# Kernel optimization log

Measured on AMD Instinct MI355X. Metric: run time of the kernel, lower is better.

The kernel has to match this reference:

```python
import jax, jax.numpy as jnp
import numpy as np

D_MODEL = 1024
D_Q = 1024
D_V = 1024


def setup_inputs() -> dict:
    key = jax.random.key(0)
    k0, k1, k2, k3 = jax.random.split(key, 4)
    embedding_word = jax.random.normal(k0, (4, 2048, D_MODEL), dtype=jnp.float32)
    # nn.Linear weights are [out, in]; we store transposed [in, out] for x @ W
    s = 1.0 / np.sqrt(D_MODEL)
    w_q = jax.random.uniform(k1, (D_MODEL, D_Q), jnp.float32, -s, s)
    w_k = jax.random.uniform(k2, (D_MODEL, D_Q), jnp.float32, -s, s)
    w_v = jax.random.uniform(k3, (D_MODEL, D_V), jnp.float32, -s, s)
    return {"embedding_word": embedding_word, "w_q": w_q, "w_k": w_k, "w_v": w_v}


def reference(embedding_word, w_q, w_k, w_v):
    # q,k: [B,T,d_q]; v: [B,T,d_v]
    q = embedding_word @ w_q
    k = embedding_word @ w_k
    v = embedding_word @ w_v
    scores = jnp.einsum("btd,bsd->bts", q, k)  # [B,T,T]
    T = scores.shape[-1]
    causal = jnp.tril(jnp.ones((T, T), dtype=bool))  # True = keep
    masked = jnp.where(causal, scores, -jnp.inf)
    weights = jax.nn.softmax(masked / jnp.sqrt(jnp.float32(D_Q)), axis=-1)
    return jnp.einsum("bts,bsv->btv", weights, v)
```

## Files before the change

kernel.cpp:

```cpp
#include <hip/hip_runtime.h>
#include <cstdint>

typedef __bf16 bf16_t;
typedef __attribute__((ext_vector_type(8))) __bf16 bf16x8;
typedef __attribute__((ext_vector_type(4))) __bf16 bf16x4;
typedef __attribute__((ext_vector_type(4))) float f32x4;

#define AS1 __attribute__((address_space(1)))
#define AS3 __attribute__((address_space(3)))

template <typename OutT>
__global__ __launch_bounds__(256)
void gemm_nt(const bf16_t* __restrict__ A, const bf16_t* __restrict__ B,
             OutT* __restrict__ C, int K, int lda, int ldb, int ldc,
             long sA, long sB, long sC, int causalSkip, int kLimit)
{
  int bm = blockIdx.y;
  const int bn = blockIdx.x;
  if (kLimit) bm = gridDim.y - 1 - bm;
  if (causalSkip && bn > bm) return;
  A += (long)blockIdx.z * sA;
  B += (long)blockIdx.z * sB;
  C += (long)blockIdx.z * sC;
  const int m0 = bm * 128, n0 = bn * 128;
  int Keff = K;
  if (kLimit) { const int kl = (bm + 1) * 128; if (kl < Keff) Keff = kl; }

  __shared__ bf16_t As[128 * 64];
  __shared__ bf16_t Bs[128 * 64];

  const int tid = threadIdx.x;
  const int wave = tid >> 6, lane = tid & 63;
  const int lm = lane & 15, qd = lane >> 4;
  const int wm = (wave >> 1) * 64, wn = (wave & 1) * 64;

  const int rowl = lane >> 3;
  const int q = (lane & 7) ^ rowl;
  const bf16_t* Abase = A + (long)(m0 + wave * 8 + rowl) * lda + q * 8;
  const bf16_t* Bbase = B + (long)(n0 + wave * 8 + rowl) * ldb + q * 8;
  bf16_t* AsW = As + wave * 512;
  bf16_t* BsW = Bs + wave * 512;

  f32x4 acc[4][4] = {};

  for (int k0 = 0; k0 < Keff; k0 += 64) {
#pragma unroll
    for (int i = 0; i < 4; i++) {
      __builtin_amdgcn_global_load_lds((const AS1 void*)(Abase + (long)i * 32 * lda + k0),
                                       (AS3 void*)(AsW + i * 2048), 16, 0, 0);
      __builtin_amdgcn_global_load_lds((const AS1 void*)(Bbase + (long)i * 32 * ldb + k0),
                                       (AS3 void*)(BsW + i * 2048), 16, 0, 0);
    }
    __syncthreads();
#pragma unroll
    for (int s = 0; s < 2; s++) {
      bf16x8 aF[4], bF[4];
#pragma unroll
      for (int i = 0; i < 4; i++) {
        const int r = wm + i * 16 + lm;
        aF[i] = *(const bf16x8*)&As[r * 64 + (((s * 4 + qd) ^ (lm & 7)) << 3)];
      }
#pragma unroll
      for (int j = 0; j < 4; j++) {
        const int r = wn + j * 16 + lm;
        bF[j] = *(const bf16x8*)&Bs[r * 64 + (((s * 4 + qd) ^ (lm & 7)) << 3)];
      }
#pragma unroll
      for (int i = 0; i < 4; i++)
#pragma unroll
        for (int j = 0; j < 4; j++)
          acc[i][j] = __builtin_amdgcn_mfma_f32_16x16x32_bf16(aF[i], bF[j], acc[i][j], 0, 0, 0);
    }
    __syncthreads();
  }

#pragma unroll
  for (int i = 0; i < 4; i++) {
    const int row = m0 + wm + i * 16 + qd * 4;
#pragma unroll
    for (int j = 0; j < 4; j++) {
      const int col = n0 + wn + j * 16 + lm;
#pragma unroll
      for (int r = 0; r < 4; r++)
        C[(long)(row + r) * ldc + col] = (OutT)acc[i][j][r];
    }
  }
}

__global__ void cvt_f32_bf16(const float* __restrict__ in, bf16_t* __restrict__ out, int n4)
{
  const int i = blockIdx.x * blockDim.x + threadIdx.x;
  if (i >= n4) return;
  const float4 f = ((const float4*)in)[i];
  bf16x4 o = {(bf16_t)f.x, (bf16_t)f.y, (bf16_t)f.z, (bf16_t)f.w};
  ((bf16x4*)out)[i] = o;
}

__global__ void cvt_transpose_w(const float* __restrict__ wq, const float* __restrict__ wk,
                                const float* __restrict__ wv, bf16_t* __restrict__ WT)
{
  const float* W = (blockIdx.z == 0) ? wq : (blockIdx.z == 1) ? wk : wv;
  bf16_t* O = WT + (long)blockIdx.z * 1024 * 1024;
  __shared__ float tile[32][33];
  const int x = blockIdx.x * 32 + threadIdx.x;
  const int y = blockIdx.y * 32 + threadIdx.y;
  tile[threadIdx.y][threadIdx.x] = W[(long)y * 1024 + x];
  __syncthreads();
  const int ox = blockIdx.x * 32 + threadIdx.y;
  const int oy = blockIdx.y * 32 + threadIdx.x;
  O[(long)ox * 1024 + oy] = (bf16_t)tile[threadIdx.x][threadIdx.y];
}

__global__ __launch_bounds__(256)
void softmax_causal(bf16_t* __restrict__ S)
{
  const int row = blockIdx.x;
  const int t = row & 2047;
  bf16_t* Sr = S + (long)row * 2048;
  const int base = threadIdx.x * 8;

  uint4 u = *(const uint4*)(Sr + base);
  const unsigned short* up = (const unsigned short*)&u;
  float v[8];
  float m = -3.0e38f;
#pragma unroll
  for (int j = 0; j < 8; j++) {
    const float x = __uint_as_float(((unsigned)up[j]) << 16);
    v[j] = (base + j <= t) ? x : -3.0e38f;
    m = fmaxf(m, v[j]);
  }
#pragma unroll
  for (int off = 32; off > 0; off >>= 1) m = fmaxf(m, __shfl_xor(m, off));
  __shared__ float redm[4], redl[4];
  const int wave = threadIdx.x >> 6, lane = threadIdx.x & 63;
  if (lane == 0) redm[wave] = m;
  __syncthreads();
  m = fmaxf(fmaxf(redm[0], redm[1]), fmaxf(redm[2], redm[3]));

  float p[8], l = 0.f;
#pragma unroll
  for (int j = 0; j < 8; j++) {
    p[j] = (base + j <= t) ? __expf((v[j] - m) * 0.03125f) : 0.f;
    l += p[j];
  }
#pragma unroll
  for (int off = 32; off > 0; off >>= 1) l += __shfl_xor(l, off);
  if (lane == 0) redl[wave] = l;
  __syncthreads();
  l = (redl[0] + redl[1]) + (redl[2] + redl[3]);
  const float rl = 1.0f / l;

  uint4 w;
  unsigned* wp = (unsigned*)&w;
#pragma unroll
  for (int h = 0; h < 4; h++) {
    bf16_t a = (bf16_t)(p[2 * h] * rl);
    bf16_t b = (bf16_t)(p[2 * h + 1] * rl);
    wp[h] = (unsigned)__builtin_bit_cast(unsigned short, a) |
            ((unsigned)__builtin_bit_cast(unsigned short, b) << 16);
  }
  *(uint4*)(Sr + base) = w;
}

extern "C" void kernel_launch(void* const* d_in, const int* in_sizes, int n_in,
                              void* d_out, int out_size, void* d_ws, size_t ws_size,
                              hipStream_t stream)
{
  const float* X  = (const float*)d_in[0];
  const float* Wq = (const float*)d_in[1];
  const float* Wk = (const float*)d_in[2];
  const float* Wv = (const float*)d_in[3];
  float* out = (float*)d_out;

  char* p = (char*)d_ws;
  bf16_t* QK = (bf16_t*)p;  p += (size_t)8192 * 2048 * 2;
  bf16_t* VT = (bf16_t*)p;  p += (size_t)1024 * 8192 * 2;
  bf16_t* WT = (bf16_t*)p;  p += (size_t)3072 * 1024 * 2;
  bf16_t* Xb = (bf16_t*)p;
  bf16_t* S  = (bf16_t*)p;

  cvt_f32_bf16<<<8192, 256, 0, stream>>>(X, Xb, 8388608 / 4);
  cvt_transpose_w<<<dim3(32, 32, 3), dim3(32, 32), 0, stream>>>(Wq, Wk, Wv, WT);
  gemm_nt<bf16_t><<<dim3(16, 64), 256, 0, stream>>>(
      Xb, WT, QK, 1024, 1024, 1024, 2048, 0, 0, 0, 0, 0);
  gemm_nt<bf16_t><<<dim3(64, 8), 256, 0, stream>>>(
      WT + (long)2048 * 1024, Xb, VT, 1024, 1024, 1024, 8192, 0, 0, 0, 0, 0);
  gemm_nt<bf16_t><<<dim3(16, 16, 4), 256, 0, stream>>>(
      QK, QK + 1024, S, 1024, 2048, 2048, 2048,
      (long)2048 * 2048, (long)2048 * 2048, (long)2048 * 2048, 1, 0);
  softmax_causal<<<8192, 256, 0, stream>>>(S);
  gemm_nt<float><<<dim3(8, 16, 4), 256, 0, stream>>>(
      S, VT, out, 2048, 2048, 8192, 1024,
      (long)2048 * 2048, 2048, (long)2048 * 1024, 0, 1);
}
```

Baseline: 264.9 us.

## Double-buffer LDS tiles in GEMM to overlap global loads with MFMA

Adds a second LDS buffer for the A and B tiles in the shared GEMM kernel. The next K-slice is prefetched with direct global-to-LDS loads while MFMAs run on the current slice, and one of the two barriers per iteration is removed. The goal is to hide global-memory latency behind compute in all four GEMMs. In exchange, LDS use per block doubles to 64 KB, which may lower the number of blocks resident per CU.

```diff
diff --git a/kernel.cpp b/kernel.cpp
--- a/kernel.cpp
+++ b/kernel.cpp
@@ -26,8 +26,8 @@
   int Keff = K;
   if (kLimit) { const int kl = (bm + 1) * 128; if (kl < Keff) Keff = kl; }
 
-  __shared__ bf16_t As[128 * 64];
-  __shared__ bf16_t Bs[128 * 64];
+  __shared__ bf16_t As[2][128 * 64];
+  __shared__ bf16_t Bs[2][128 * 64];
 
   const int tid = threadIdx.x;
   const int wave = tid >> 6, lane = tid & 63;
@@ -38,32 +38,38 @@
   const int q = (lane & 7) ^ rowl;
   const bf16_t* Abase = A + (long)(m0 + wave * 8 + rowl) * lda + q * 8;
   const bf16_t* Bbase = B + (long)(n0 + wave * 8 + rowl) * ldb + q * 8;
-  bf16_t* AsW = As + wave * 512;
-  bf16_t* BsW = Bs + wave * 512;
+  const int woff = wave * 512;
+
+#define STAGE(K0, BUF)                                                        \
+  _Pragma("unroll")                                                           \
+  for (int i = 0; i < 4; i++) {                                               \
+    __builtin_amdgcn_global_load_lds(                                         \
+        (const AS1 void*)(Abase + (long)i * 32 * lda + (K0)),                 \
+        (AS3 void*)(As[BUF] + woff + i * 2048), 16, 0, 0);                    \
+    __builtin_amdgcn_global_load_lds(                                         \
+        (const AS1 void*)(Bbase + (long)i * 32 * ldb + (K0)),                 \
+        (AS3 void*)(Bs[BUF] + woff + i * 2048), 16, 0, 0);                    \
+  }
 
   f32x4 acc[4][4] = {};
 
+  STAGE(0, 0);
+  int buf = 0;
   for (int k0 = 0; k0 < Keff; k0 += 64) {
-#pragma unroll
-    for (int i = 0; i < 4; i++) {
-      __builtin_amdgcn_global_load_lds((const AS1 void*)(Abase + (long)i * 32 * lda + k0),
-                                       (AS3 void*)(AsW + i * 2048), 16, 0, 0);
-      __builtin_amdgcn_global_load_lds((const AS1 void*)(Bbase + (long)i * 32 * ldb + k0),
-                                       (AS3 void*)(BsW + i * 2048), 16, 0, 0);
-    }
     __syncthreads();
+    if (k0 + 64 < Keff) { STAGE(k0 + 64, buf ^ 1); }
 #pragma unroll
     for (int s = 0; s < 2; s++) {
       bf16x8 aF[4], bF[4];
 #pragma unroll
       for (int i = 0; i < 4; i++) {
         const int r = wm + i * 16 + lm;
-        aF[i] = *(const bf16x8*)&As[r * 64 + (((s * 4 + qd) ^ (lm & 7)) << 3)];
+        aF[i] = *(const bf16x8*)&As[buf][r * 64 + (((s * 4 + qd) ^ (lm & 7)) << 3)];
       }
 #pragma unroll
       for (int j = 0; j < 4; j++) {
         const int r = wn + j * 16 + lm;
-        bF[j] = *(const bf16x8*)&Bs[r * 64 + (((s * 4 + qd) ^ (lm & 7)) << 3)];
+        bF[j] = *(const bf16x8*)&Bs[buf][r * 64 + (((s * 4 + qd) ^ (lm & 7)) << 3)];
       }
 #pragma unroll
       for (int i = 0; i < 4; i++)
@@ -71,8 +77,9 @@
         for (int j = 0; j < 4; j++)
           acc[i][j] = __builtin_amdgcn_mfma_f32_16x16x32_bf16(aF[i], bF[j], acc[i][j], 0, 0, 0);
     }
-    __syncthreads();
-  }
+    buf ^= 1;
+  }
+#undef STAGE
 
 #pragma unroll
   for (int i = 0; i < 4; i++) {
```

Result: faster. 253.2 us (-4.4%).
